# Optimization experiments

Hardware: AMD Instinct MI355X
Metric: run time of the kernel (lower is better)

The kernel has to match this reference:

```python
import jax, jax.numpy as jnp
import numpy as np

D_HEAD = 64

def setup_inputs() -> dict:
    key = jax.random.key(0)
    kq, kk, kv, km = jax.random.split(key, 4)
    B, H, S, D = 4, 16, 2048, D_HEAD
    q = jax.random.normal(kq, (B, H, S, D), dtype=jnp.float32)
    k = jax.random.normal(kk, (B, H, S, D), dtype=jnp.float32)
    v = jax.random.normal(kv, (B, H, S, D), dtype=jnp.float32)
    mask = jax.random.randint(km, (B, 1, S, S), 0, 2, dtype=jnp.int32)
    return {"q": q, "k": k, "v": v, "mask": mask}

def reference(q, k, v, mask):
    # scores: [B,H,S,S]
    scores = jnp.einsum('bhqd,bhkd->bhqk', q, k) / jnp.sqrt(jnp.asarray(D_HEAD, q.dtype))
    neg_inf = jnp.asarray(-jnp.inf, scores.dtype)
    scores = jnp.where(mask == 0, neg_inf, scores)
    attn = jax.nn.softmax(scores, axis=-1)
    # dropout is identity in eval mode (deterministic reference)
    return jnp.einsum('bhqk,bhkd->bhqd', attn, v)
```

## Files before the change

kernel.cpp:

```cpp
#include <hip/hip_runtime.h>


constexpr int Bc = 4, Hc = 16, Sc = 2048, Dc = 64;
constexpr int QBLK = 256, KVBLK = 64;
constexpr int NT = Sc / KVBLK;

typedef _Float16 half8 __attribute__((ext_vector_type(8)));
typedef _Float16 half4 __attribute__((ext_vector_type(4)));
typedef _Float16 half2v __attribute__((ext_vector_type(2)));
typedef __fp16  fp16x2 __attribute__((ext_vector_type(2)));
typedef float floatx4 __attribute__((ext_vector_type(4)));

#define GLB(p) ((const __attribute__((address_space(1))) void*)(p))
#define LDSP(p) ((__attribute__((address_space(3))) void*)(p))

union U32F2 { unsigned int u; fp16x2 h; };
union U32H2 { unsigned int u; half2v h; };
union PFRAG { unsigned int u[4]; half8 h; };

__device__ inline float dot2acc(unsigned int pu, float acc) {
#if __has_builtin(__builtin_amdgcn_fdot2)
    U32H2 c; c.u = pu;
    half2v ones2 = { (_Float16)1.0f, (_Float16)1.0f };
    return __builtin_amdgcn_fdot2(c.h, ones2, acc, false);
#else
    U32H2 c; c.u = pu;
    return acc + (float)c.h[0] + (float)c.h[1];
#endif
}

__global__ __launch_bounds__(256) void mask_to_bits(
    const int* __restrict__ M, unsigned long long* __restrict__ W)
{
    size_t i = (size_t)blockIdx.x * 256 + threadIdx.x;
    int v = M[i];
    unsigned long long bal = __ballot(v != 0);
    if ((threadIdx.x & 63) == 0) W[i >> 6] = bal;
}

__global__ __launch_bounds__(256) void mask_to_bytes(
    const int* __restrict__ M, unsigned int* __restrict__ M8)
{
    size_t t = (size_t)blockIdx.x * 256 + threadIdx.x;
    const int4* src = (const int4*)M + t * 4;
    uint4 out;
    unsigned int* o = (unsigned int*)&out;
    #pragma unroll
    for (int w = 0; w < 4; ++w) {
        int4 v = src[w];
        o[w] = (v.x ? 0xFFu : 0u) | (v.y ? 0xFF00u : 0u) |
               (v.z ? 0xFF0000u : 0u) | (v.w ? 0xFF000000u : 0u);
    }
    ((uint4*)M8)[t] = out;
}

__global__ __launch_bounds__(256) void kv_convert_v4(
    const float* __restrict__ Kp, const float* __restrict__ Vp,
    unsigned char* __restrict__ K16, unsigned char* __restrict__ V16)
{
    __shared__ float vlds[64][65];
    const int tid = threadIdx.x;
    const int kt  = blockIdx.x;
    const int bh  = blockIdx.y;
    const int kv0 = kt * 64;
    const float* ksrc = Kp + ((size_t)bh * Sc + kv0) * Dc;
    const float* vsrc = Vp + ((size_t)bh * Sc + kv0) * Dc;
    unsigned char* kdst = K16 + (size_t)bh * Sc * 128 + (size_t)kv0 * 128;
    unsigned char* vdst = V16 + (size_t)bh * Sc * 128 + (size_t)kv0 * 128;

    #pragma unroll
    for (int it = 0; it < 4; ++it) {
        int idx = it * 256 + tid;
        int o   = idx >> 4;
        int d0  = (idx & 15) * 4;
        float4 kval = *(const float4*)(ksrc + o * Dc + d0);
        half4 kh;
        kh[0] = (_Float16)kval.x; kh[1] = (_Float16)kval.y;
        kh[2] = (_Float16)kval.z; kh[3] = (_Float16)kval.w;
        int r = ((o >> 2) & 3) * 16 + ((o >> 4) << 2) + (o & 3);
        *(half4*)(kdst + r * 128 + ((d0 * 2) ^ ((r & 7) << 4))) = kh;

        float4 vval = *(const float4*)(vsrc + o * Dc + d0);
        vlds[o][d0]     = vval.x;
        vlds[o][d0 + 1] = vval.y;
        vlds[o][d0 + 2] = vval.z;
        vlds[o][d0 + 3] = vval.w;
    }
    __syncthreads();
    #pragma unroll
    for (int i = 0; i < 2; ++i) {
        int ch  = i * 256 + tid;
        int l15 = ch & 15;
        int lg  = (ch >> 4) & 3;
        int c   = (ch >> 6) & 1;
        int nd  = ch >> 7;
        int d   = nd * 16 + l15;
        half8 h;
        #pragma unroll
        for (int w = 0; w < 4; ++w) {
            int kvlog = lg * 16 + (2 * c + (w >> 1)) * 4 + (w & 1) * 2;
            h[w * 2]     = (_Float16)vlds[kvlog][d];
            h[w * 2 + 1] = (_Float16)vlds[kvlog + 1][d];
        }
        *(half8*)(vdst + ch * 16) = h;
    }
}

template <int MMODE>
__global__ __launch_bounds__(512) void attn_v11(
    const float* __restrict__ Qp,
    const unsigned char* __restrict__ K16, const unsigned char* __restrict__ V16,
    const unsigned char* __restrict__ M8, const unsigned long long* __restrict__ Wb,
    float* __restrict__ Op)
{
    __shared__ __align__(16) unsigned char lds[49152];

    const int tid  = threadIdx.x;
    const int w    = tid >> 6;
    const int lane = tid & 63;
    const int l15  = lane & 15;
    const int lg   = lane >> 4;

    const int ib      = blockIdx.x;
    const int logical = (ib & 7) * 64 + (ib >> 3);
    const int qt = logical & 7;
    const int bh = logical >> 3;
    const int b  = bh >> 4;
    const int q0 = qt * QBLK + w * 32 + l15;
    const int q1 = q0 + 16;

    const size_t qkv_base = (size_t)bh * Sc * Dc;
    const unsigned char* k16src = K16 + (size_t)bh * Sc * 128;
    const unsigned char* v16src = V16 + (size_t)bh * Sc * 128;
    const unsigned char* mp0 = M8 + (size_t)b * Sc * Sc + (size_t)q0 * Sc + lg * 16;
    const unsigned char* mp1 = mp0 + (size_t)16 * Sc;
    const unsigned long long* wr0 = Wb + ((size_t)b * Sc + q0) * (Sc / 64);
    const unsigned long long* wr1 = Wb + ((size_t)b * Sc + q1) * (Sc / 64);

    const float qscale = 0.125f * 1.44269504088896f;
    half8 qfrag[2][2];
    #pragma unroll
    for (int qg = 0; qg < 2; ++qg) {
        const float* qrow = Qp + qkv_base + (size_t)(qg ? q1 : q0) * Dc;
        #pragma unroll
        for (int c = 0; c < 2; ++c) {
            int d0 = c * 32 + lg * 8;
            float4 qa = *(const float4*)(qrow + d0);
            float4 qb = *(const float4*)(qrow + d0 + 4);
            qfrag[qg][c][0] = (_Float16)(qa.x * qscale);
            qfrag[qg][c][1] = (_Float16)(qa.y * qscale);
            qfrag[qg][c][2] = (_Float16)(qa.z * qscale);
            qfrag[qg][c][3] = (_Float16)(qa.w * qscale);
            qfrag[qg][c][4] = (_Float16)(qb.x * qscale);
            qfrag[qg][c][5] = (_Float16)(qb.y * qscale);
            qfrag[qg][c][6] = (_Float16)(qb.z * qscale);
            qfrag[qg][c][7] = (_Float16)(qb.w * qscale);
        }
    }

    floatx4 o_acc[2][4];
    float   l_run[2] = {0.f, 0.f};
    #pragma unroll
    for (int qg = 0; qg < 2; ++qg)
        #pragma unroll
        for (int n = 0; n < 4; ++n) o_acc[qg][n] = (floatx4)0.f;

    const int ldsOff = w * 1024;
    const unsigned char* kg = k16src + ldsOff + lane * 16;
    const unsigned char* vg = v16src + ldsOff + lane * 16;

    uint4 mk[3][2];
    unsigned long long wk[3][2];

    auto STAGE = [&](int slot) {
        __builtin_amdgcn_global_load_lds(GLB(kg), LDSP(lds + slot * 16384 + ldsOff),        16, 0, 0);
        __builtin_amdgcn_global_load_lds(GLB(vg), LDSP(lds + slot * 16384 + 8192 + ldsOff), 16, 0, 0);
        kg += 8192; vg += 8192;
    };
    auto LOADM = [&](int slot) {
        if (MMODE == 0) {
            mk[slot][0] = *(const uint4*)(mp0); mp0 += KVBLK;
            mk[slot][1] = *(const uint4*)(mp1); mp1 += KVBLK;
        } else {
            wk[slot][0] = *wr0; ++wr0;
            wk[slot][1] = *wr1; ++wr1;
        }
    };

    auto COMP = [&](int j) {
        const unsigned char* kbase = lds + j * 16384;
        const unsigned char* vbase = lds + j * 16384 + 8192;

        floatx4 s[2][4];
        __builtin_amdgcn_s_setprio(1);
        #pragma unroll
        for (int n = 0; n < 4; ++n) {
            const unsigned char* krow = kbase + (n * 16 + l15) * 128;
            half8 kf0 = *(const half8*)(krow + ((lg * 16)      ^ ((l15 & 7) << 4)));
            half8 kf1 = *(const half8*)(krow + ((64 + lg * 16) ^ ((l15 & 7) << 4)));
            floatx4 a0 = __builtin_amdgcn_mfma_f32_16x16x32_f16(kf0, qfrag[0][0], (floatx4)0.f, 0, 0, 0);
            a0 = __builtin_amdgcn_mfma_f32_16x16x32_f16(kf1, qfrag[0][1], a0, 0, 0, 0);
            floatx4 a1 = __builtin_amdgcn_mfma_f32_16x16x32_f16(kf0, qfrag[1][0], (floatx4)0.f, 0, 0, 0);
            a1 = __builtin_amdgcn_mfma_f32_16x16x32_f16(kf1, qfrag[1][1], a1, 0, 0, 0);
            s[0][n] = a0;
            s[1][n] = a1;
        }
        __builtin_amdgcn_s_setprio(0);

        PFRAG pf[2][2];
        #pragma unroll
        for (int qg = 0; qg < 2; ++qg) {
            unsigned int nib16;
            if (MMODE == 1) {
                unsigned long long wc = wk[j][qg];
                unsigned int lo = (unsigned int)wc, hi = (unsigned int)(wc >> 32);
                unsigned int half = (lg & 2) ? hi : lo;
                nib16 = (lg & 1) ? (half >> 16) : (half & 0xFFFFu);
            }
            const unsigned int* mw = (const unsigned int*)&mk[j][qg];
            float rs = l_run[qg];
            #pragma unroll
            for (int n = 0; n < 4; ++n) {
                float p0 = __builtin_amdgcn_exp2f(s[qg][n][0]);
                float p1 = __builtin_amdgcn_exp2f(s[qg][n][1]);
                float p2 = __builtin_amdgcn_exp2f(s[qg][n][2]);
                float p3 = __builtin_amdgcn_exp2f(s[qg][n][3]);
                U32F2 h01, h23;
                h01.h = __builtin_amdgcn_cvt_pkrtz(p0, p1);
                h23.h = __builtin_amdgcn_cvt_pkrtz(p2, p3);
                unsigned int msk0, msk1;
                if (MMODE == 0) {
                    msk0 = __builtin_amdgcn_perm(0u, mw[n], 0x01010000u);
                    msk1 = __builtin_amdgcn_perm(0u, mw[n], 0x03030202u);
                } else {
                    unsigned int x0 = nib16 >> (n * 4);
                    unsigned int x1 = nib16 >> (n * 4 + 2);
                    msk0 = ((x0 & 1u) | ((x0 & 2u) << 15)) * 0xFFFFu;
                    msk1 = ((x1 & 1u) | ((x1 & 2u) << 15)) * 0xFFFFu;
                }
                unsigned int w0 = h01.u & msk0;
                unsigned int w1 = h23.u & msk1;
                pf[qg][n >> 1].u[(n & 1) * 2]     = w0;
                pf[qg][n >> 1].u[(n & 1) * 2 + 1] = w1;
                rs = dot2acc(w0, rs);
                rs = dot2acc(w1, rs);
            }
            l_run[qg] = rs;
        }

        __builtin_amdgcn_s_setprio(1);
        #pragma unroll
        for (int nd = 0; nd < 4; ++nd) {
            const unsigned char* vrow = vbase + ((nd * 8 + lg) * 16 + l15) * 16;
            half8 vf0 = *(const half8*)(vrow);
            half8 vf1 = *(const half8*)(vrow + 1024);
            o_acc[0][nd] = __builtin_amdgcn_mfma_f32_16x16x32_f16(vf0, pf[0][0].h, o_acc[0][nd], 0, 0, 0);
            o_acc[0][nd] = __builtin_amdgcn_mfma_f32_16x16x32_f16(vf1, pf[0][1].h, o_acc[0][nd], 0, 0, 0);
            o_acc[1][nd] = __builtin_amdgcn_mfma_f32_16x16x32_f16(vf0, pf[1][0].h, o_acc[1][nd], 0, 0, 0);
            o_acc[1][nd] = __builtin_amdgcn_mfma_f32_16x16x32_f16(vf1, pf[1][1].h, o_acc[1][nd], 0, 0, 0);
        }
        __builtin_amdgcn_s_setprio(0);
    };

    STAGE(0); LOADM(0);
    STAGE(1); LOADM(1);

    for (int i = 0; i < 10; ++i) {
        #pragma unroll
        for (int j = 0; j < 3; ++j) {
            asm volatile("s_waitcnt vmcnt(4)" ::: "memory");
            __builtin_amdgcn_s_barrier();
            STAGE((j + 2) % 3);
            LOADM((j + 2) % 3);
            COMP(j);
        }
    }
    asm volatile("s_waitcnt vmcnt(4)" ::: "memory");
    __builtin_amdgcn_s_barrier();
    COMP(0);
    asm volatile("s_waitcnt vmcnt(0)" ::: "memory");
    __builtin_amdgcn_s_barrier();
    COMP(1);

    #pragma unroll
    for (int qg = 0; qg < 2; ++qg) {
        float r = l_run[qg];
        r += __shfl_xor(r, 16);
        r += __shfl_xor(r, 32);
        float inv_l = 1.0f / r;
        float* orow = Op + qkv_base + (size_t)(qg ? q1 : q0) * Dc;
        #pragma unroll
        for (int nd = 0; nd < 4; ++nd) {
            float4 st;
            st.x = o_acc[qg][nd][0] * inv_l;
            st.y = o_acc[qg][nd][1] * inv_l;
            st.z = o_acc[qg][nd][2] * inv_l;
            st.w = o_acc[qg][nd][3] * inv_l;
            *(float4*)(orow + nd * 16 + lg * 4) = st;
        }
    }
}

template <bool USE_BITS>
__global__ __launch_bounds__(256) void attn_old(
    const float* __restrict__ Qp, const float* __restrict__ Kp,
    const float* __restrict__ Vp, const int* __restrict__ Mp,
    const unsigned long long* __restrict__ Wb, float* __restrict__ Op)
{
    __shared__ __align__(16) unsigned char lds[24576];
    const int tid  = threadIdx.x;
    const int w    = tid >> 6;
    const int lane = tid & 63;
    const int l15  = lane & 15;
    const int lg   = lane >> 4;
    const int qt = blockIdx.x;
    const int bh = blockIdx.y;
    const int b  = bh >> 4;
    const int qbase = qt * 64;
    const size_t qkv_base = (size_t)bh * Sc * Dc;
    const int*   mrow     = Mp + (size_t)b * Sc * Sc;
    const unsigned long long* wrow =
        Wb + ((size_t)b * Sc + qbase + w * 16 + lg * 4) * (Sc / 64);

    const float qscale = 0.125f * 1.44269504088896f;
    half8 qfrag[2];
    {
        const float* qrow = Qp + qkv_base + (size_t)(qbase + w * 16 + l15) * Dc;
        #pragma unroll
        for (int c = 0; c < 2; ++c) {
            int d0 = c * 32 + lg * 8;
            float4 qa = *(const float4*)(qrow + d0);
            float4 qb = *(const float4*)(qrow + d0 + 4);
            #pragma unroll
            for (int e = 0; e < 4; ++e) qfrag[c][e] = (_Float16)(((const float*)&qa)[e] * qscale);
            #pragma unroll
            for (int e = 0; e < 4; ++e) qfrag[c][4 + e] = (_Float16)(((const float*)&qb)[e] * qscale);
        }
    }
    float m_run[4], l_run[4];
    floatx4 o_acc[4];
    #pragma unroll
    for (int j = 0; j < 4; ++j) { m_run[j] = -1e30f; l_run[j] = 0.f; }
    #pragma unroll
    for (int n = 0; n < 4; ++n) o_acc[n] = (floatx4)0.f;

    for (int kv0 = 0; kv0 < Sc; kv0 += 64) {
        __syncthreads();
        {
            const float* ksrc = Kp + qkv_base + (size_t)kv0 * Dc;
            const float* vsrc = Vp + qkv_base + (size_t)kv0 * Dc;
            #pragma unroll
            for (int it = 0; it < 4; ++it) {
                int idx = it * 256 + tid;
                int kv  = idx >> 4;
                int d0  = (idx & 15) * 4;
                float4 kval = *(const float4*)(ksrc + kv * Dc + d0);
                half4 kh;
                kh[0] = (_Float16)kval.x; kh[1] = (_Float16)kval.y;
                kh[2] = (_Float16)kval.z; kh[3] = (_Float16)kval.w;
                *(half4*)(lds + ((kv * 128 + d0 * 2) ^ ((kv & 7) << 4))) = kh;
                float4 vval = *(const float4*)(vsrc + kv * Dc + d0);
                float vv[4] = { vval.x, vval.y, vval.z, vval.w };
                #pragma unroll
                for (int i = 0; i < 4; ++i) {
                    int d = d0 + i;
                    *(_Float16*)(lds + 8192 + ((d * 128 + kv * 2) ^ ((d & 7) << 4))) = (_Float16)vv[i];
                }
            }
        }
        __syncthreads();

        unsigned int mlo[4], mhi[4];
        if (USE_BITS) {
            #pragma unroll
            for (int j = 0; j < 4; ++j) {
                unsigned long long mw = wrow[(size_t)j * (Sc / 64) + (kv0 >> 6)];
                mlo[j] = (unsigned int)mw;
                mhi[j] = (unsigned int)(mw >> 32);
            }
        }
        floatx4 s[4];
        #pragma unroll
        for (int n = 0; n < 4; ++n) {
            floatx4 acc = (floatx4)0.f;
            #pragma unroll
            for (int c = 0; c < 2; ++c) {
                int kvr = n * 16 + l15;
                int d0  = c * 32 + lg * 8;
                half8 bfrag = *(const half8*)(lds + ((kvr * 128 + d0 * 2) ^ ((kvr & 7) << 4)));
                acc = __builtin_amdgcn_mfma_f32_16x16x32_f16(qfrag[c], bfrag, acc, 0, 0, 0);
            }
            s[n] = acc;
        }
        float tmax[4];
        #pragma unroll
        for (int j = 0; j < 4; ++j) tmax[j] = -1e30f;
        #pragma unroll
        for (int n = 0; n < 4; ++n) {
            #pragma unroll
            for (int j = 0; j < 4; ++j) {
                unsigned int bit;
                if (USE_BITS) {
                    unsigned int word = (n < 2) ? mlo[j] : mhi[j];
                    bit = (word >> (((n & 1) << 4) + l15)) & 1u;
                } else {
                    int qr  = qbase + w * 16 + lg * 4 + j;
                    int kvc = kv0 + n * 16 + l15;
                    bit = (mrow[(size_t)qr * Sc + kvc] != 0) ? 1u : 0u;
                }
                float sv = bit ? s[n][j] : -1e30f;
                s[n][j] = sv;
                tmax[j] = fmaxf(tmax[j], sv);
            }
        }
        #pragma unroll
        for (int j = 0; j < 4; ++j) {
            float tv = tmax[j];
            tv = fmaxf(tv, __shfl_xor(tv, 1));
            tv = fmaxf(tv, __shfl_xor(tv, 2));
            tv = fmaxf(tv, __shfl_xor(tv, 4));
            tv = fmaxf(tv, __shfl_xor(tv, 8));
            tmax[j] = tv;
        }
        float corr[4], rsum[4];
        #pragma unroll
        for (int j = 0; j < 4; ++j) {
            float mnew = fmaxf(m_run[j], tmax[j]);
            corr[j] = exp2f(m_run[j] - mnew);
            m_run[j] = mnew;
            rsum[j] = 0.f;
        }
        unsigned char* pbase = lds + 16384 + w * 2048;
        #pragma unroll
        for (int n = 0; n < 4; ++n) {
            #pragma unroll
            for (int j = 0; j < 4; ++j) {
                float p = exp2f(s[n][j] - m_run[j]);
                rsum[j] += p;
                int off = ((lg * 4 + j) * 128 + (n * 16 + l15) * 2) ^ (((lg * 4 + j) & 7) << 4);
                *(_Float16*)(pbase + off) = (_Float16)p;
            }
        }
        #pragma unroll
        for (int j = 0; j < 4; ++j) {
            float r = rsum[j];
            r += __shfl_xor(r, 1);
            r += __shfl_xor(r, 2);
            r += __shfl_xor(r, 4);
            r += __shfl_xor(r, 8);
            l_run[j] = l_run[j] * corr[j] + r;
        }
        #pragma unroll
        for (int n = 0; n < 4; ++n)
            #pragma unroll
            for (int j = 0; j < 4; ++j)
                o_acc[n][j] *= corr[j];

        half8 pfrag[2];
        #pragma unroll
        for (int c = 0; c < 2; ++c) {
            int kvc = c * 32 + lg * 8;
            pfrag[c] = *(const half8*)(pbase + ((l15 * 128 + kvc * 2) ^ ((l15 & 7) << 4)));
        }
        #pragma unroll
        for (int n = 0; n < 4; ++n) {
            #pragma unroll
            for (int c = 0; c < 2; ++c) {
                int d   = n * 16 + l15;
                int kvc = c * 32 + lg * 8;
                half8 vfrag = *(const half8*)(lds + 8192 + ((d * 128 + kvc * 2) ^ ((d & 7) << 4)));
                o_acc[n] = __builtin_amdgcn_mfma_f32_16x16x32_f16(pfrag[c], vfrag, o_acc[n], 0, 0, 0);
            }
        }
    }
    float inv_l[4];
    #pragma unroll
    for (int j = 0; j < 4; ++j) inv_l[j] = 1.0f / l_run[j];
    float* obase = Op + qkv_base;
    #pragma unroll
    for (int n = 0; n < 4; ++n)
        #pragma unroll
        for (int j = 0; j < 4; ++j)
            obase[(size_t)(qbase + w * 16 + lg * 4 + j) * Dc + n * 16 + l15] = o_acc[n][j] * inv_l[j];
}

extern "C" void kernel_launch(void* const* d_in, const int* in_sizes, int n_in,
                              void* d_out, int out_size, void* d_ws, size_t ws_size,
                              hipStream_t stream) {
    const float* Q = (const float*)d_in[0];
    const float* K = (const float*)d_in[1];
    const float* V = (const float*)d_in[2];
    const int*   M = (const int*)d_in[3];
    float*       O = (float*)d_out;

    const int nblk = (Sc / QBLK) * Bc * Hc;
    const size_t SZ_BITS = (size_t)Bc * Sc * (Sc / 64) * 8;
    const size_t SZ_K    = (size_t)Bc * Hc * Sc * 128;
    const size_t SZ_V    = SZ_K;
    const size_t SZ_M8   = (size_t)Bc * Sc * Sc;

    if (ws_size >= SZ_K + SZ_V + SZ_M8) {
        unsigned char* K16 = (unsigned char*)d_ws;
        unsigned char* V16 = K16 + SZ_K;
        unsigned char* M8  = V16 + SZ_V;
        mask_to_bytes<<<(Bc * Sc * Sc) / (256 * 16), 256, 0, stream>>>(M, (unsigned int*)M8);
        kv_convert_v4<<<dim3(Sc / 64, Bc * Hc), 256, 0, stream>>>(K, V, K16, V16);
        attn_v11<0><<<nblk, 512, 0, stream>>>(Q, K16, V16, M8, nullptr, O);
    } else if (ws_size >= SZ_BITS + SZ_K + SZ_V) {
        unsigned long long* W = (unsigned long long*)d_ws;
        unsigned char* K16 = (unsigned char*)d_ws + SZ_BITS;
        unsigned char* V16 = K16 + SZ_K;
        mask_to_bits<<<(Bc * Sc * Sc) / 256, 256, 0, stream>>>(M, W);
        kv_convert_v4<<<dim3(Sc / 64, Bc * Hc), 256, 0, stream>>>(K, V, K16, V16);
        attn_v11<1><<<nblk, 512, 0, stream>>>(Q, K16, V16, nullptr, W, O);
    } else if (ws_size >= SZ_BITS) {
        unsigned long long* W = (unsigned long long*)d_ws;
        mask_to_bits<<<(Bc * Sc * Sc) / 256, 256, 0, stream>>>(M, W);
        attn_old<true><<<dim3(Sc / 64, Bc * Hc), 256, 0, stream>>>(Q, K, V, M, W, O);
    } else {
        attn_old<false><<<dim3(Sc / 64, Bc * Hc), 256, 0, stream>>>(Q, K, V, M, nullptr, O);
    }
}
```

Baseline: 119.0 us.

## Process 64 query rows per wave with 256-thread blocks and bitmask-only path

The attention kernel now uses 4 waves per block, each handling 64 query rows (four 16-row groups) instead of 32, so every K/V fragment read from LDS feeds twice as many MFMAs. The byte-mask path and its conversion kernel are removed, and the bit-packed mask is always used, which cuts mask traffic. QK^T, exp and masking are interleaved per query group. Each thread holds more registers (four query groups of accumulators and fragments), and there are fewer waves per block to hide latency.

```diff
diff --git a/kernel.cpp b/kernel.cpp
--- a/kernel.cpp
+++ b/kernel.cpp
@@ -36,22 +36,6 @@
     int v = M[i];
     unsigned long long bal = __ballot(v != 0);
     if ((threadIdx.x & 63) == 0) W[i >> 6] = bal;
-}
-
-__global__ __launch_bounds__(256) void mask_to_bytes(
-    const int* __restrict__ M, unsigned int* __restrict__ M8)
-{
-    size_t t = (size_t)blockIdx.x * 256 + threadIdx.x;
-    const int4* src = (const int4*)M + t * 4;
-    uint4 out;
-    unsigned int* o = (unsigned int*)&out;
-    #pragma unroll
-    for (int w = 0; w < 4; ++w) {
-        int4 v = src[w];
-        o[w] = (v.x ? 0xFFu : 0u) | (v.y ? 0xFF00u : 0u) |
-               (v.z ? 0xFF0000u : 0u) | (v.w ? 0xFF000000u : 0u);
-    }
-    ((uint4*)M8)[t] = out;
 }
 
 __global__ __launch_bounds__(256) void kv_convert_v4(
@@ -106,12 +90,10 @@
     }
 }
 
-template <int MMODE>
-__global__ __launch_bounds__(512) void attn_v11(
+__global__ __launch_bounds__(256) void attn_v14(
     const float* __restrict__ Qp,
     const unsigned char* __restrict__ K16, const unsigned char* __restrict__ V16,
-    const unsigned char* __restrict__ M8, const unsigned long long* __restrict__ Wb,
-    float* __restrict__ Op)
+    const unsigned long long* __restrict__ Wb, float* __restrict__ Op)
 {
     __shared__ __align__(16) unsigned char lds[49152];
 
@@ -126,22 +108,18 @@
     const int qt = logical & 7;
     const int bh = logical >> 3;
     const int b  = bh >> 4;
-    const int q0 = qt * QBLK + w * 32 + l15;
-    const int q1 = q0 + 16;
+    const int q0 = qt * QBLK + w * 64 + l15;
 
     const size_t qkv_base = (size_t)bh * Sc * Dc;
     const unsigned char* k16src = K16 + (size_t)bh * Sc * 128;
     const unsigned char* v16src = V16 + (size_t)bh * Sc * 128;
-    const unsigned char* mp0 = M8 + (size_t)b * Sc * Sc + (size_t)q0 * Sc + lg * 16;
-    const unsigned char* mp1 = mp0 + (size_t)16 * Sc;
-    const unsigned long long* wr0 = Wb + ((size_t)b * Sc + q0) * (Sc / 64);
-    const unsigned long long* wr1 = Wb + ((size_t)b * Sc + q1) * (Sc / 64);
+    const unsigned long long* wrt = Wb + ((size_t)b * Sc + q0) * (Sc / 64);
 
     const float qscale = 0.125f * 1.44269504088896f;
-    half8 qfrag[2][2];
-    #pragma unroll
-    for (int qg = 0; qg < 2; ++qg) {
-        const float* qrow = Qp + qkv_base + (size_t)(qg ? q1 : q0) * Dc;
+    half8 qfrag[4][2];
+    #pragma unroll
+    for (int qg = 0; qg < 4; ++qg) {
+        const float* qrow = Qp + qkv_base + (size_t)(q0 + qg * 16) * Dc;
         #pragma unroll
         for (int c = 0; c < 2; ++c) {
             int d0 = c * 32 + lg * 8;
@@ -158,95 +136,81 @@
         }
     }
 
-    floatx4 o_acc[2][4];
-    float   l_run[2] = {0.f, 0.f};
-    #pragma unroll
-    for (int qg = 0; qg < 2; ++qg)
+    floatx4 o_acc[4][4];
+    float   l_run[4] = {0.f, 0.f, 0.f, 0.f};
+    #pragma unroll
+    for (int qg = 0; qg < 4; ++qg)
         #pragma unroll
         for (int n = 0; n < 4; ++n) o_acc[qg][n] = (floatx4)0.f;
 
-    const int ldsOff = w * 1024;
+    const int ldsOff = (w * 2) * 1024;
     const unsigned char* kg = k16src + ldsOff + lane * 16;
     const unsigned char* vg = v16src + ldsOff + lane * 16;
 
-    uint4 mk[3][2];
-    unsigned long long wk[3][2];
+    unsigned long long wk[3][4];
 
     auto STAGE = [&](int slot) {
-        __builtin_amdgcn_global_load_lds(GLB(kg), LDSP(lds + slot * 16384 + ldsOff),        16, 0, 0);
-        __builtin_amdgcn_global_load_lds(GLB(vg), LDSP(lds + slot * 16384 + 8192 + ldsOff), 16, 0, 0);
+        __builtin_amdgcn_global_load_lds(GLB(kg),        LDSP(lds + slot * 16384 + ldsOff),               16, 0, 0);
+        __builtin_amdgcn_global_load_lds(GLB(kg + 1024), LDSP(lds + slot * 16384 + ldsOff + 1024),        16, 0, 0);
+        __builtin_amdgcn_global_load_lds(GLB(vg),        LDSP(lds + slot * 16384 + 8192 + ldsOff),        16, 0, 0);
+        __builtin_amdgcn_global_load_lds(GLB(vg + 1024), LDSP(lds + slot * 16384 + 8192 + ldsOff + 1024), 16, 0, 0);
         kg += 8192; vg += 8192;
     };
     auto LOADM = [&](int slot) {
-        if (MMODE == 0) {
-            mk[slot][0] = *(const uint4*)(mp0); mp0 += KVBLK;
-            mk[slot][1] = *(const uint4*)(mp1); mp1 += KVBLK;
-        } else {
-            wk[slot][0] = *wr0; ++wr0;
-            wk[slot][1] = *wr1; ++wr1;
-        }
+        wk[slot][0] = wrt[0];
+        wk[slot][1] = wrt[512];
+        wk[slot][2] = wrt[1024];
+        wk[slot][3] = wrt[1536];
+        ++wrt;
     };
 
     auto COMP = [&](int j) {
         const unsigned char* kbase = lds + j * 16384;
         const unsigned char* vbase = lds + j * 16384 + 8192;
 
-        floatx4 s[2][4];
-        __builtin_amdgcn_s_setprio(1);
+        unsigned int nib16[4];
+        #pragma unroll
+        for (int qg = 0; qg < 4; ++qg) {
+            unsigned long long wc = wk[j][qg];
+            unsigned int lo = (unsigned int)wc, hi = (unsigned int)(wc >> 32);
+            unsigned int half = (lg & 2) ? hi : lo;
+            nib16[qg] = (lg & 1) ? (half >> 16) : (half & 0xFFFFu);
+        }
+
+        PFRAG pf[4][2];
+        float rs0 = l_run[0], rs1 = l_run[1], rs2 = l_run[2], rs3 = l_run[3];
         #pragma unroll
         for (int n = 0; n < 4; ++n) {
             const unsigned char* krow = kbase + (n * 16 + l15) * 128;
             half8 kf0 = *(const half8*)(krow + ((lg * 16)      ^ ((l15 & 7) << 4)));
             half8 kf1 = *(const half8*)(krow + ((64 + lg * 16) ^ ((l15 & 7) << 4)));
-            floatx4 a0 = __builtin_amdgcn_mfma_f32_16x16x32_f16(kf0, qfrag[0][0], (floatx4)0.f, 0, 0, 0);
-            a0 = __builtin_amdgcn_mfma_f32_16x16x32_f16(kf1, qfrag[0][1], a0, 0, 0, 0);
-            floatx4 a1 = __builtin_amdgcn_mfma_f32_16x16x32_f16(kf0, qfrag[1][0], (floatx4)0.f, 0, 0, 0);
-            a1 = __builtin_amdgcn_mfma_f32_16x16x32_f16(kf1, qfrag[1][1], a1, 0, 0, 0);
-            s[0][n] = a0;
-            s[1][n] = a1;
-        }
-        __builtin_amdgcn_s_setprio(0);
-
-        PFRAG pf[2][2];
-        #pragma unroll
-        for (int qg = 0; qg < 2; ++qg) {
-            unsigned int nib16;
-            if (MMODE == 1) {
-                unsigned long long wc = wk[j][qg];
-                unsigned int lo = (unsigned int)wc, hi = (unsigned int)(wc >> 32);
-                unsigned int half = (lg & 2) ? hi : lo;
-                nib16 = (lg & 1) ? (half >> 16) : (half & 0xFFFFu);
-            }
-            const unsigned int* mw = (const unsigned int*)&mk[j][qg];
-            float rs = l_run[qg];
-            #pragma unroll
-            for (int n = 0; n < 4; ++n) {
-                float p0 = __builtin_amdgcn_exp2f(s[qg][n][0]);
-                float p1 = __builtin_amdgcn_exp2f(s[qg][n][1]);
-                float p2 = __builtin_amdgcn_exp2f(s[qg][n][2]);
-                float p3 = __builtin_amdgcn_exp2f(s[qg][n][3]);
+            #pragma unroll
+            for (int qg = 0; qg < 4; ++qg) {
+                floatx4 a = __builtin_amdgcn_mfma_f32_16x16x32_f16(kf0, qfrag[qg][0], (floatx4)0.f, 0, 0, 0);
+                a = __builtin_amdgcn_mfma_f32_16x16x32_f16(kf1, qfrag[qg][1], a, 0, 0, 0);
+                float p0 = __builtin_amdgcn_exp2f(a[0]);
+                float p1 = __builtin_amdgcn_exp2f(a[1]);
+                float p2 = __builtin_amdgcn_exp2f(a[2]);
+                float p3 = __builtin_amdgcn_exp2f(a[3]);
                 U32F2 h01, h23;
                 h01.h = __builtin_amdgcn_cvt_pkrtz(p0, p1);
                 h23.h = __builtin_amdgcn_cvt_pkrtz(p2, p3);
-                unsigned int msk0, msk1;
-                if (MMODE == 0) {
-                    msk0 = __builtin_amdgcn_perm(0u, mw[n], 0x01010000u);
-                    msk1 = __builtin_amdgcn_perm(0u, mw[n], 0x03030202u);
-                } else {
-                    unsigned int x0 = nib16 >> (n * 4);
-                    unsigned int x1 = nib16 >> (n * 4 + 2);
-                    msk0 = ((x0 & 1u) | ((x0 & 2u) << 15)) * 0xFFFFu;
-                    msk1 = ((x1 & 1u) | ((x1 & 2u) << 15)) * 0xFFFFu;
-                }
+                unsigned int x0 = nib16[qg] >> (n * 4);
+                unsigned int x1 = nib16[qg] >> (n * 4 + 2);
+                unsigned int msk0 = ((x0 & 1u) | ((x0 & 2u) << 15)) * 0xFFFFu;
+                unsigned int msk1 = ((x1 & 1u) | ((x1 & 2u) << 15)) * 0xFFFFu;
                 unsigned int w0 = h01.u & msk0;
                 unsigned int w1 = h23.u & msk1;
                 pf[qg][n >> 1].u[(n & 1) * 2]     = w0;
                 pf[qg][n >> 1].u[(n & 1) * 2 + 1] = w1;
+                float rs = (qg == 0) ? rs0 : (qg == 1) ? rs1 : (qg == 2) ? rs2 : rs3;
                 rs = dot2acc(w0, rs);
                 rs = dot2acc(w1, rs);
-            }
-            l_run[qg] = rs;
-        }
+                if (qg == 0) rs0 = rs; else if (qg == 1) rs1 = rs;
+                else if (qg == 2) rs2 = rs; else rs3 = rs;
+            }
+        }
+        l_run[0] = rs0; l_run[1] = rs1; l_run[2] = rs2; l_run[3] = rs3;
 
         __builtin_amdgcn_s_setprio(1);
         #pragma unroll
@@ -254,10 +218,11 @@
             const unsigned char* vrow = vbase + ((nd * 8 + lg) * 16 + l15) * 16;
             half8 vf0 = *(const half8*)(vrow);
             half8 vf1 = *(const half8*)(vrow + 1024);
-            o_acc[0][nd] = __builtin_amdgcn_mfma_f32_16x16x32_f16(vf0, pf[0][0].h, o_acc[0][nd], 0, 0, 0);
-            o_acc[0][nd] = __builtin_amdgcn_mfma_f32_16x16x32_f16(vf1, pf[0][1].h, o_acc[0][nd], 0, 0, 0);
-            o_acc[1][nd] = __builtin_amdgcn_mfma_f32_16x16x32_f16(vf0, pf[1][0].h, o_acc[1][nd], 0, 0, 0);
-            o_acc[1][nd] = __builtin_amdgcn_mfma_f32_16x16x32_f16(vf1, pf[1][1].h, o_acc[1][nd], 0, 0, 0);
+            #pragma unroll
+            for (int qg = 0; qg < 4; ++qg) {
+                o_acc[qg][nd] = __builtin_amdgcn_mfma_f32_16x16x32_f16(vf0, pf[qg][0].h, o_acc[qg][nd], 0, 0, 0);
+                o_acc[qg][nd] = __builtin_amdgcn_mfma_f32_16x16x32_f16(vf1, pf[qg][1].h, o_acc[qg][nd], 0, 0, 0);
+            }
         }
         __builtin_amdgcn_s_setprio(0);
     };
@@ -268,14 +233,14 @@
     for (int i = 0; i < 10; ++i) {
         #pragma unroll
         for (int j = 0; j < 3; ++j) {
-            asm volatile("s_waitcnt vmcnt(4)" ::: "memory");
+            asm volatile("s_waitcnt vmcnt(8)" ::: "memory");
             __builtin_amdgcn_s_barrier();
             STAGE((j + 2) % 3);
             LOADM((j + 2) % 3);
             COMP(j);
         }
     }
-    asm volatile("s_waitcnt vmcnt(4)" ::: "memory");
+    asm volatile("s_waitcnt vmcnt(8)" ::: "memory");
     __builtin_amdgcn_s_barrier();
     COMP(0);
     asm volatile("s_waitcnt vmcnt(0)" ::: "memory");
@@ -283,12 +248,12 @@
     COMP(1);
 
     #pragma unroll
-    for (int qg = 0; qg < 2; ++qg) {
+    for (int qg = 0; qg < 4; ++qg) {
         float r = l_run[qg];
         r += __shfl_xor(r, 16);
         r += __shfl_xor(r, 32);
         float inv_l = 1.0f / r;
-        float* orow = Op + qkv_base + (size_t)(qg ? q1 : q0) * Dc;
+        float* orow = Op + qkv_base + (size_t)(q0 + qg * 16) * Dc;
         #pragma unroll
         for (int nd = 0; nd < 4; ++nd) {
             float4 st;
@@ -497,22 +462,14 @@
     const size_t SZ_BITS = (size_t)Bc * Sc * (Sc / 64) * 8;
     const size_t SZ_K    = (size_t)Bc * Hc * Sc * 128;
     const size_t SZ_V    = SZ_K;
-    const size_t SZ_M8   = (size_t)Bc * Sc * Sc;
-
-    if (ws_size >= SZ_K + SZ_V + SZ_M8) {
-        unsigned char* K16 = (unsigned char*)d_ws;
-        unsigned char* V16 = K16 + SZ_K;
-        unsigned char* M8  = V16 + SZ_V;
-        mask_to_bytes<<<(Bc * Sc * Sc) / (256 * 16), 256, 0, stream>>>(M, (unsigned int*)M8);
-        kv_convert_v4<<<dim3(Sc / 64, Bc * Hc), 256, 0, stream>>>(K, V, K16, V16);
-        attn_v11<0><<<nblk, 512, 0, stream>>>(Q, K16, V16, M8, nullptr, O);
-    } else if (ws_size >= SZ_BITS + SZ_K + SZ_V) {
+
+    if (ws_size >= SZ_BITS + SZ_K + SZ_V) {
         unsigned long long* W = (unsigned long long*)d_ws;
         unsigned char* K16 = (unsigned char*)d_ws + SZ_BITS;
         unsigned char* V16 = K16 + SZ_K;
         mask_to_bits<<<(Bc * Sc * Sc) / 256, 256, 0, stream>>>(M, W);
         kv_convert_v4<<<dim3(Sc / 64, Bc * Hc), 256, 0, stream>>>(K, V, K16, V16);
-        attn_v11<1><<<nblk, 512, 0, stream>>>(Q, K16, V16, nullptr, W, O);
+        attn_v14<<<nblk, 256, 0, stream>>>(Q, K16, V16, W, O);
     } else if (ws_size >= SZ_BITS) {
         unsigned long long* W = (unsigned long long*)d_ws;
         mask_to_bits<<<(Bc * Sc * Sc) / 256, 256, 0, stream>>>(M, W);
```

Result: slower. 160.7 us (+35.0%).
